# Kernel tuning notes

Hardware: AMD Instinct MI355X
Metric: run time of the kernel (lower is better)

The kernel has to match this reference:

```python
import jax, jax.numpy as jnp
import numpy as np

N, E, F_IN, H, D = 50000, 800000, 128, 4, 32


def setup_inputs() -> dict:
    key = jax.random.key(0)
    k_x, k_e, k_w, k_al, k_ar = jax.random.split(key, 5)
    x = jax.random.normal(k_x, (N, F_IN), dtype=jnp.float32)
    edge_index = jax.random.randint(k_e, (2, E), 0, N, dtype=jnp.int32).astype(jnp.int64)
    # xavier-uniform-like scales
    s_w = float(np.sqrt(6.0 / (F_IN + H * D)))
    s_a = float(np.sqrt(6.0 / (D + 1)))
    W = jax.random.uniform(k_w, (F_IN, H * D), jnp.float32, -s_w, s_w)
    att_l = jax.random.uniform(k_al, (H, D), jnp.float32, -s_a, s_a)
    att_r = jax.random.uniform(k_ar, (H, D), jnp.float32, -s_a, s_a)
    bias = jnp.zeros((H * D,), jnp.float32)
    return {"x": x, "edge_index": edge_index, "W": W, "att_l": att_l, "att_r": att_r, "bias": bias}


def reference(x, edge_index, W, att_l, att_r, bias):
    num_nodes = x.shape[0]
    n_heads, head_dim = att_l.shape
    h = (x @ W).reshape(num_nodes, n_heads, head_dim)          # [N,H,D]
    alpha_l = jnp.einsum('nhd,hd->nh', h, att_l)               # [N,H]
    alpha_r = jnp.einsum('nhd,hd->nh', h, att_r)               # [N,H]
    from_idx, to_idx = edge_index[0], edge_index[1]
    att = alpha_l[from_idx] + alpha_r[to_idx]                  # [E,H]
    att = jax.nn.leaky_relu(att, negative_slope=0.2)
    # segment softmax over edges grouped by destination node (shift by global
    # per-head max, exactly as the source's _softmax effectively does)
    att = att - jax.lax.stop_gradient(jnp.max(att, axis=0, keepdims=True))
    ex = jnp.exp(att)                                          # [E,H]
    denom = jax.ops.segment_sum(ex, to_idx, num_segments=num_nodes)  # [N,H]
    att_n = ex / (denom[to_idx] + 1e-9)                        # [E,H]
    # scatter-weighted aggregation: out[n] = sum_{e: to=n} att[e] * h[from[e]]
    msgs = att_n[:, :, None] * h[from_idx]                     # [E,H,D]
    out = jax.ops.segment_sum(msgs, to_idx, num_segments=num_nodes)  # [N,H,D]
    out = out.reshape(num_nodes, n_heads * head_dim) + bias
    return out
```

## Files before the change

kernel.cpp:

```cpp
#include <hip/hip_runtime.h>
#include <cstdint>

#define N_NODES 50000
#define N_EDGES 800000
#define F_IN    128
#define N_HEADS 4
#define HEAD_DIM 32
#define F_OUT   128

#define NBUCK   196
#define KA_GRID 256
#define EPB     (N_EDGES / KA_GRID)
#define CAPA    64
#define STAGE_CAP 6144

typedef unsigned int uint32;
typedef unsigned short ushort;
typedef __attribute__((ext_vector_type(8))) short short8v;
typedef __attribute__((ext_vector_type(4))) float float4v;

__device__ __forceinline__ ushort f2bf(float f) {
    uint32 u = __float_as_uint(f);
    return (ushort)((u + 0x7FFFu + ((u >> 16) & 1u)) >> 16);
}

__device__ __forceinline__ int block_scan_excl_256(int v, int* p_total)
{
    const int t = threadIdx.x, lane = t & 63, wv = t >> 6;
    int incl = v;
#pragma unroll
    for (int d = 1; d < 64; d <<= 1) {
        int u = __shfl_up(incl, d);
        if (lane >= d) incl += u;
    }
    __shared__ int wsum[4];
    if (lane == 63) wsum[wv] = incl;
    __syncthreads();
    int woff = 0;
#pragma unroll
    for (int j = 0; j < 4; ++j) {
        int s = wsum[j];
        if (j < wv) woff += s;
    }
    if (p_total) *p_total = wsum[0] + wsum[1] + wsum[2] + wsum[3];
    __syncthreads();
    return woff + incl - v;
}

__global__ __launch_bounds__(256) void k_bin(const int* __restrict__ ei,
    const float* __restrict__ W, ushort* __restrict__ WT_hi,
    ushort* __restrict__ WT_lo, uint2* __restrict__ priv, int* __restrict__ cnts)
{
    const int sb = blockIdx.x, t = threadIdx.x;

    const int id = sb * 256 + t;
    if (id < F_IN * F_OUT) {
        const int n = id & 127, k = id >> 7;
        const float w = W[k * F_OUT + n];
        const ushort hi = f2bf(w);
        const float hif = __uint_as_float((uint32)hi << 16);
        WT_hi[n * F_IN + k] = hi;
        WT_lo[n * F_IN + k] = f2bf(w - hif);
    }

    __shared__ int cur[NBUCK];
    if (t < NBUCK) cur[t] = 0;
    __syncthreads();

    const int e0 = sb * EPB;
    for (int i = t; i < EPB; i += 256) {
        const int from = ei[e0 + i];
        const int to   = ei[N_EDGES + e0 + i];
        const int b = to >> 8;
        const int slot = atomicAdd(&cur[b], 1);
        if (slot < CAPA)
            priv[((size_t)b * KA_GRID + sb) * CAPA + slot] =
                make_uint2((uint32)from, (uint32)to);
    }
    __syncthreads();
    if (t < NBUCK) cnts[t * KA_GRID + sb] = min(cur[t], CAPA);
}

__global__ __launch_bounds__(256) void k_bsum(const int* __restrict__ cnts,
                                              int* __restrict__ bsum)
{
    const int b = blockIdx.x, t = threadIdx.x;
    int v = cnts[b * KA_GRID + t];
#pragma unroll
    for (int d = 32; d; d >>= 1) v += __shfl_xor(v, d);
    __shared__ int ws[4];
    if ((t & 63) == 0) ws[t >> 6] = v;
    __syncthreads();
    if (t == 0) bsum[b] = ws[0] + ws[1] + ws[2] + ws[3];
}

__global__ __launch_bounds__(256) void k_scan_base(const int* __restrict__ bsum,
    int* __restrict__ bucket_base)
{
    const int t = threadIdx.x;
    int v = (t < NBUCK) ? bsum[t] : 0;
    const int ex = block_scan_excl_256(v, nullptr);
    if (t < NBUCK) bucket_base[t] = ex;
}

__global__ __launch_bounds__(256) void k_build(const uint2* __restrict__ priv,
    const int* __restrict__ cnts, const int* __restrict__ bucket_base,
    int* __restrict__ count, int* __restrict__ offsets, int* __restrict__ rec_from)
{
    __shared__ uint2 stage[STAGE_CAP];
    __shared__ int hist[256];
    __shared__ int curn[256];
    const int b = blockIdx.x, t = threadIdx.x;

    const int ct = cnts[b * KA_GRID + t];
    int total;
    const int so = block_scan_excl_256(ct, &total);

    const uint2* seg = priv + ((size_t)b * KA_GRID + t) * CAPA;
    if (so + ct <= STAGE_CAP)
        for (int i = 0; i < ct; ++i) stage[so + i] = seg[i];
    hist[t] = 0;
    __syncthreads();

    const int S = min(total, STAGE_CAP);
    for (int i = t; i < S; i += 256) atomicAdd(&hist[stage[i].y & 255], 1);
    __syncthreads();

    const int hv = hist[t];
    int tot2;
    const int lo = block_scan_excl_256(hv, &tot2);
    const int base = bucket_base[b];
    const int n = b * 256 + t;
    if (n < N_NODES) {
        count[n]   = hv;
        offsets[n] = base + lo;
    }
    curn[t] = lo;
    __syncthreads();

    for (int i = t; i < S; i += 256) {
        const uint2 e = stage[i];
        const int pos = atomicAdd(&curn[e.y & 255], 1);
        rec_from[base + pos] = (int)e.x;
    }
}

__global__ __launch_bounds__(256) void k_gemm_mfma(
    const float* __restrict__ x,
    const ushort* __restrict__ WT_hi, const ushort* __restrict__ WT_lo,
    const float* __restrict__ attl, const float* __restrict__ attr,
    uint32* __restrict__ hbp, float* __restrict__ aLp, float* __restrict__ aRp)
{
    const int lane = threadIdx.x & 63;
    const int wv   = threadIdx.x >> 6;
    const int q    = lane >> 4;
    const int c15  = lane & 15;
    const int row0 = blockIdx.x * 64 + wv * 16;
    if (row0 >= N_NODES) return;

    const float* xrow = x + (size_t)(row0 + c15) * F_IN + q * 8;
    short8v ahi[4], alo[4];
#pragma unroll
    for (int kt = 0; kt < 4; ++kt) {
        const float4 f0 = *(const float4*)(xrow + kt * 32);
        const float4 f1 = *(const float4*)(xrow + kt * 32 + 4);
        const float fs[8] = {f0.x, f0.y, f0.z, f0.w, f1.x, f1.y, f1.z, f1.w};
#pragma unroll
        for (int j = 0; j < 8; ++j) {
            const ushort hi = f2bf(fs[j]);
            const float hif = __uint_as_float((uint32)hi << 16);
            ahi[kt][j] = (short)hi;
            alo[kt][j] = (short)f2bf(fs[j] - hif);
        }
    }

    float4v acc[8];
#pragma unroll
    for (int nt = 0; nt < 8; ++nt) {
        float4v a = {0.f, 0.f, 0.f, 0.f};
        const ushort* bh_base = WT_hi + ((nt * 16 + c15) << 7) + q * 8;
        const ushort* bl_base = WT_lo + ((nt * 16 + c15) << 7) + q * 8;
#pragma unroll
        for (int kt = 0; kt < 4; ++kt) {
            const short8v bh = *(const short8v*)(bh_base + kt * 32);
            const short8v bl = *(const short8v*)(bl_base + kt * 32);
            a = __builtin_amdgcn_mfma_f32_16x16x32_bf16(ahi[kt], bh, a, 0, 0, 0);
            a = __builtin_amdgcn_mfma_f32_16x16x32_bf16(alo[kt], bh, a, 0, 0, 0);
            a = __builtin_amdgcn_mfma_f32_16x16x32_bf16(ahi[kt], bl, a, 0, 0, 0);
        }
        acc[nt] = a;
    }

#pragma unroll
    for (int nt = 0; nt < 4; ++nt) {
#pragma unroll
        for (int r = 0; r < 4; ++r) {
            const uint32 d = (uint32)f2bf(acc[nt][r]) | ((uint32)f2bf(acc[nt + 4][r]) << 16);
            hbp[(size_t)(row0 + q * 4 + r) * 64 + nt * 16 + c15] = d;
        }
    }

    float aLacc[4][4] = {{0.f}}, aRacc[4][4] = {{0.f}};
#pragma unroll
    for (int nt = 0; nt < 8; ++nt) {
        const float alv = attl[nt * 16 + c15];
        const float arv = attr[nt * 16 + c15];
        const int hh = nt >> 1;
#pragma unroll
        for (int r = 0; r < 4; ++r) {
            aLacc[r][hh] = fmaf(acc[nt][r], alv, aLacc[r][hh]);
            aRacc[r][hh] = fmaf(acc[nt][r], arv, aRacc[r][hh]);
        }
    }
#pragma unroll
    for (int r = 0; r < 4; ++r) {
#pragma unroll
        for (int hh = 0; hh < 4; ++hh) {
            float vl = aLacc[r][hh], vr = aRacc[r][hh];
#pragma unroll
            for (int d = 1; d < 16; d <<= 1) {
                vl += __shfl_xor(vl, d);
                vr += __shfl_xor(vr, d);
            }
            if (c15 == hh) {
                const int row = row0 + q * 4 + r;
                const int pos = (hh & 1) * 2 + (hh >> 1);
                aLp[row * N_HEADS + pos] = vl;
                aRp[row * N_HEADS + pos] = vr;
            }
        }
    }
}

__global__ __launch_bounds__(256) void k_agg(const int* __restrict__ rec_from,
    const int* __restrict__ count, const int* __restrict__ offsets,
    const float* __restrict__ aLp, const float* __restrict__ aRp,
    const uint32* __restrict__ hbp,
    const float* __restrict__ bias, float* __restrict__ out)
{
    const int lane = threadIdx.x & 63;
    const int n = blockIdx.x * 4 + (threadIdx.x >> 6);
    if (n >= N_NODES) return;
    const int cnt  = count[n];
    const int off  = offsets[n];
    const int hsel = (lane >> 5) * 2;
    const int l31  = lane & 31;
    const int gsel = lane & 32;
    const float2 arv = *(const float2*)&aRp[n * N_HEADS + hsel];
    float ax = 0.f, ay = 0.f, ds0 = 0.f, ds1 = 0.f;

    for (int base = 0; base < cnt; base += 32) {
        const int m = min(32, cnt - base);
        int vf = 0;
        float e0p = 0.f, e1p = 0.f;
        if (l31 < m) {
            vf = rec_from[off + base + l31];
            const float2 af = *(const float2*)&aLp[vf * N_HEADS + hsel];
            float t0 = af.x + arv.x; t0 = (t0 > 0.f) ? t0 : 0.2f * t0;
            float t1 = af.y + arv.y; t1 = (t1 > 0.f) ? t1 : 0.2f * t1;
            e0p = __expf(t0);
            e1p = __expf(t1);
        }
        int i = 0;
        for (; i + 4 <= m; i += 4) {
            const int s0 = gsel | i, s1 = gsel | (i + 1);
            const int s2 = gsel | (i + 2), s3 = gsel | (i + 3);
            const int f0 = __shfl(vf, s0), f1 = __shfl(vf, s1);
            const int f2i = __shfl(vf, s2), f3 = __shfl(vf, s3);
            const uint32 h0 = hbp[(size_t)f0 * 64 + lane];
            const uint32 h1 = hbp[(size_t)f1 * 64 + lane];
            const uint32 h2 = hbp[(size_t)f2i * 64 + lane];
            const uint32 h3 = hbp[(size_t)f3 * 64 + lane];
            const float e00 = __shfl(e0p, s0), e10 = __shfl(e1p, s0);
            const float e01 = __shfl(e0p, s1), e11 = __shfl(e1p, s1);
            const float e02 = __shfl(e0p, s2), e12 = __shfl(e1p, s2);
            const float e03 = __shfl(e0p, s3), e13 = __shfl(e1p, s3);
            ax = fmaf(e00, __uint_as_float(h0 << 16), ax);
            ay = fmaf(e10, __uint_as_float(h0 & 0xFFFF0000u), ay);
            ds0 += e00; ds1 += e10;
            ax = fmaf(e01, __uint_as_float(h1 << 16), ax);
            ay = fmaf(e11, __uint_as_float(h1 & 0xFFFF0000u), ay);
            ds0 += e01; ds1 += e11;
            ax = fmaf(e02, __uint_as_float(h2 << 16), ax);
            ay = fmaf(e12, __uint_as_float(h2 & 0xFFFF0000u), ay);
            ds0 += e02; ds1 += e12;
            ax = fmaf(e03, __uint_as_float(h3 << 16), ax);
            ay = fmaf(e13, __uint_as_float(h3 & 0xFFFF0000u), ay);
            ds0 += e03; ds1 += e13;
        }
        for (; i < m; ++i) {
            const int s = gsel | i;
            const int f = __shfl(vf, s);
            const uint32 hv = hbp[(size_t)f * 64 + lane];
            const float e0 = __shfl(e0p, s), e1 = __shfl(e1p, s);
            ax = fmaf(e0, __uint_as_float(hv << 16), ax);
            ay = fmaf(e1, __uint_as_float(hv & 0xFFFF0000u), ay);
            ds0 += e0; ds1 += e1;
        }
    }
    const float inv0 = 1.0f / (ds0 + 1e-9f);
    const float inv1 = 1.0f / (ds1 + 1e-9f);
    out[n * F_OUT + lane]      = ax * inv0 + bias[lane];
    out[n * F_OUT + 64 + lane] = ay * inv1 + bias[64 + lane];
}

extern "C" void kernel_launch(void* const* d_in, const int* in_sizes, int n_in,
                              void* d_out, int out_size, void* d_ws, size_t ws_size,
                              hipStream_t stream)
{
    const float* x    = (const float*)d_in[0];
    const int*   ei   = (const int*)d_in[1];
    const float* W    = (const float*)d_in[2];
    const float* attl = (const float*)d_in[3];
    const float* attr = (const float*)d_in[4];
    const float* bias = (const float*)d_in[5];
    float* out = (float*)d_out;

    char* p = (char*)d_ws;
    auto carve = [&](size_t bytes) -> char* {
        char* q = p;
        p += (bytes + 255) & ~size_t(255);
        return q;
    };
    uint32* hbp       = (uint32*)carve((size_t)N_NODES * 64 * 4);
    uint2*  priv      = (uint2*)carve((size_t)NBUCK * KA_GRID * CAPA * 8);
    int*    rec_from  = (int*)carve((size_t)N_EDGES * 4);
    ushort* WT_hi     = (ushort*)carve((size_t)F_IN * F_OUT * 2);
    ushort* WT_lo     = (ushort*)carve((size_t)F_IN * F_OUT * 2);
    float*  aLp       = (float*)carve((size_t)N_NODES * N_HEADS * 4);
    float*  aRp       = (float*)carve((size_t)N_NODES * N_HEADS * 4);
    int*    cnts      = (int*)carve((size_t)NBUCK * KA_GRID * 4);
    int*    bsum      = (int*)carve(NBUCK * 4);
    int*    bucket_base = (int*)carve(NBUCK * 4);
    int*    count     = (int*)carve((size_t)N_NODES * 4);
    int*    offsets   = (int*)carve((size_t)N_NODES * 4);

    k_bin<<<KA_GRID, 256, 0, stream>>>(ei, W, WT_hi, WT_lo, priv, cnts);
    k_bsum<<<NBUCK, 256, 0, stream>>>(cnts, bsum);
    k_scan_base<<<1, 256, 0, stream>>>(bsum, bucket_base);
    k_build<<<NBUCK, 256, 0, stream>>>(priv, cnts, bucket_base,
                                       count, offsets, rec_from);
    k_gemm_mfma<<<(N_NODES + 63) / 64, 256, 0, stream>>>(x, WT_hi, WT_lo,
                                                         attl, attr, hbp, aLp, aRp);
    k_agg<<<(N_NODES + 3) / 4, 256, 0, stream>>>(rec_from, count, offsets,
                                                 aLp, aRp, hbp, bias, out);
}
```

Baseline: 181.3 us.

## Split GEMM column halves across waves, coalesce staging copy, repack h layout

In k_build, the per-thread serial copy of each private edge segment into shared memory becomes a block-strided loop, so consecutive threads read consecutive priv entries and the loads coalesce. The GEMM kernel now gives each 16-row strip to two waves, each computing half the output columns (two heads). This doubles the grid and halves accumulator registers per wave. The packed bf16 h layout changes to match, and the aggregation kernel's output indexing and the attention-logit slot order are adjusted to fit. The cost is that each x strip is loaded and converted twice and there is more index arithmetic.

```diff
diff --git a/kernel.cpp b/kernel.cpp
--- a/kernel.cpp
+++ b/kernel.cpp
@@ -110,16 +110,27 @@
     __shared__ uint2 stage[STAGE_CAP];
     __shared__ int hist[256];
     __shared__ int curn[256];
+    __shared__ int so_s[256];
+    __shared__ int cts_s[256];
     const int b = blockIdx.x, t = threadIdx.x;
 
     const int ct = cnts[b * KA_GRID + t];
     int total;
     const int so = block_scan_excl_256(ct, &total);
-
-    const uint2* seg = priv + ((size_t)b * KA_GRID + t) * CAPA;
-    if (so + ct <= STAGE_CAP)
-        for (int i = 0; i < ct; ++i) stage[so + i] = seg[i];
+    so_s[t] = so;
+    cts_s[t] = ct;
     hist[t] = 0;
+    __syncthreads();
+
+    const uint2* pbase = priv + (size_t)b * KA_GRID * CAPA;
+    for (int idx = t; idx < KA_GRID * CAPA; idx += 256) {
+        const int sb = idx >> 6;
+        const int sl = idx & (CAPA - 1);
+        if (sl < cts_s[sb]) {
+            const int p = so_s[sb] + sl;
+            if (p < STAGE_CAP) stage[p] = pbase[idx];
+        }
+    }
     __syncthreads();
 
     const int S = min(total, STAGE_CAP);
@@ -149,13 +160,15 @@
     const float* __restrict__ x,
     const ushort* __restrict__ WT_hi, const ushort* __restrict__ WT_lo,
     const float* __restrict__ attl, const float* __restrict__ attr,
-    uint32* __restrict__ hbp, float* __restrict__ aLp, float* __restrict__ aRp)
-{
-    const int lane = threadIdx.x & 63;
-    const int wv   = threadIdx.x >> 6;
-    const int q    = lane >> 4;
-    const int c15  = lane & 15;
-    const int row0 = blockIdx.x * 64 + wv * 16;
+    uint32* __restrict__ hbq, float* __restrict__ aLp, float* __restrict__ aRp)
+{
+    const int lane  = threadIdx.x & 63;
+    const int wv    = threadIdx.x >> 6;
+    const int strip = blockIdx.x * 2 + (wv >> 1);
+    const int half  = wv & 1;
+    const int q     = lane >> 4;
+    const int c15   = lane & 15;
+    const int row0  = strip * 16;
     if (row0 >= N_NODES) return;
 
     const float* xrow = x + (size_t)(row0 + c15) * F_IN + q * 8;
@@ -174,9 +187,10 @@
         }
     }
 
-    float4v acc[8];
-#pragma unroll
-    for (int nt = 0; nt < 8; ++nt) {
+    float4v acc[4];
+#pragma unroll
+    for (int j = 0; j < 4; ++j) {
+        const int nt = half * 4 + j;
         float4v a = {0.f, 0.f, 0.f, 0.f};
         const ushort* bh_base = WT_hi + ((nt * 16 + c15) << 7) + q * 8;
         const ushort* bl_base = WT_lo + ((nt * 16 + c15) << 7) + q * 8;
@@ -188,45 +202,45 @@
             a = __builtin_amdgcn_mfma_f32_16x16x32_bf16(alo[kt], bh, a, 0, 0, 0);
             a = __builtin_amdgcn_mfma_f32_16x16x32_bf16(ahi[kt], bl, a, 0, 0, 0);
         }
-        acc[nt] = a;
-    }
-
-#pragma unroll
-    for (int nt = 0; nt < 4; ++nt) {
+        acc[j] = a;
+    }
+
+#pragma unroll
+    for (int j = 0; j < 2; ++j) {
 #pragma unroll
         for (int r = 0; r < 4; ++r) {
-            const uint32 d = (uint32)f2bf(acc[nt][r]) | ((uint32)f2bf(acc[nt + 4][r]) << 16);
-            hbp[(size_t)(row0 + q * 4 + r) * 64 + nt * 16 + c15] = d;
-        }
-    }
-
-    float aLacc[4][4] = {{0.f}}, aRacc[4][4] = {{0.f}};
-#pragma unroll
-    for (int nt = 0; nt < 8; ++nt) {
-        const float alv = attl[nt * 16 + c15];
-        const float arv = attr[nt * 16 + c15];
-        const int hh = nt >> 1;
+            const uint32 d = (uint32)f2bf(acc[j][r]) | ((uint32)f2bf(acc[j + 2][r]) << 16);
+            hbq[(size_t)(row0 + q * 4 + r) * 64 + half * 32 + j * 16 + c15] = d;
+        }
+    }
+
+    float aLacc[4][2] = {{0.f}}, aRacc[4][2] = {{0.f}};
+#pragma unroll
+    for (int j = 0; j < 4; ++j) {
+        const int col = (half * 4 + j) * 16 + c15;
+        const float alv = attl[col];
+        const float arv = attr[col];
+        const int hl = j >> 1;
 #pragma unroll
         for (int r = 0; r < 4; ++r) {
-            aLacc[r][hh] = fmaf(acc[nt][r], alv, aLacc[r][hh]);
-            aRacc[r][hh] = fmaf(acc[nt][r], arv, aRacc[r][hh]);
+            aLacc[r][hl] = fmaf(acc[j][r], alv, aLacc[r][hl]);
+            aRacc[r][hl] = fmaf(acc[j][r], arv, aRacc[r][hl]);
         }
     }
 #pragma unroll
     for (int r = 0; r < 4; ++r) {
 #pragma unroll
-        for (int hh = 0; hh < 4; ++hh) {
-            float vl = aLacc[r][hh], vr = aRacc[r][hh];
+        for (int hl = 0; hl < 2; ++hl) {
+            float vl = aLacc[r][hl], vr = aRacc[r][hl];
 #pragma unroll
             for (int d = 1; d < 16; d <<= 1) {
                 vl += __shfl_xor(vl, d);
                 vr += __shfl_xor(vr, d);
             }
-            if (c15 == hh) {
+            if (c15 == hl) {
                 const int row = row0 + q * 4 + r;
-                const int pos = (hh & 1) * 2 + (hh >> 1);
-                aLp[row * N_HEADS + pos] = vl;
-                aRp[row * N_HEADS + pos] = vr;
+                aLp[row * N_HEADS + half * 2 + hl] = vl;
+                aRp[row * N_HEADS + half * 2 + hl] = vr;
             }
         }
     }
@@ -235,7 +249,7 @@
 __global__ __launch_bounds__(256) void k_agg(const int* __restrict__ rec_from,
     const int* __restrict__ count, const int* __restrict__ offsets,
     const float* __restrict__ aLp, const float* __restrict__ aRp,
-    const uint32* __restrict__ hbp,
+    const uint32* __restrict__ hbq,
     const float* __restrict__ bias, float* __restrict__ out)
 {
     const int lane = threadIdx.x & 63;
@@ -267,10 +281,10 @@
             const int s2 = gsel | (i + 2), s3 = gsel | (i + 3);
             const int f0 = __shfl(vf, s0), f1 = __shfl(vf, s1);
             const int f2i = __shfl(vf, s2), f3 = __shfl(vf, s3);
-            const uint32 h0 = hbp[(size_t)f0 * 64 + lane];
-            const uint32 h1 = hbp[(size_t)f1 * 64 + lane];
-            const uint32 h2 = hbp[(size_t)f2i * 64 + lane];
-            const uint32 h3 = hbp[(size_t)f3 * 64 + lane];
+            const uint32 h0 = hbq[(size_t)f0 * 64 + lane];
+            const uint32 h1 = hbq[(size_t)f1 * 64 + lane];
+            const uint32 h2 = hbq[(size_t)f2i * 64 + lane];
+            const uint32 h3 = hbq[(size_t)f3 * 64 + lane];
             const float e00 = __shfl(e0p, s0), e10 = __shfl(e1p, s0);
             const float e01 = __shfl(e0p, s1), e11 = __shfl(e1p, s1);
             const float e02 = __shfl(e0p, s2), e12 = __shfl(e1p, s2);
@@ -291,7 +305,7 @@
         for (; i < m; ++i) {
             const int s = gsel | i;
             const int f = __shfl(vf, s);
-            const uint32 hv = hbp[(size_t)f * 64 + lane];
+            const uint32 hv = hbq[(size_t)f * 64 + lane];
             const float e0 = __shfl(e0p, s), e1 = __shfl(e1p, s);
             ax = fmaf(e0, __uint_as_float(hv << 16), ax);
             ay = fmaf(e1, __uint_as_float(hv & 0xFFFF0000u), ay);
@@ -300,8 +314,9 @@
     }
     const float inv0 = 1.0f / (ds0 + 1e-9f);
     const float inv1 = 1.0f / (ds1 + 1e-9f);
-    out[n * F_OUT + lane]      = ax * inv0 + bias[lane];
-    out[n * F_OUT + 64 + lane] = ay * inv1 + bias[64 + lane];
+    const int d0 = (lane < 32) ? lane : lane + 32;
+    out[n * F_OUT + d0]      = ax * inv0 + bias[d0];
+    out[n * F_OUT + d0 + 32] = ay * inv1 + bias[d0 + 32];
 }
 
 extern "C" void kernel_launch(void* const* d_in, const int* in_sizes, int n_in,
@@ -322,7 +337,7 @@
         p += (bytes + 255) & ~size_t(255);
         return q;
     };
-    uint32* hbp       = (uint32*)carve((size_t)N_NODES * 64 * 4);
+    uint32* hbq       = (uint32*)carve((size_t)N_NODES * 64 * 4);
     uint2*  priv      = (uint2*)carve((size_t)NBUCK * KA_GRID * CAPA * 8);
     int*    rec_from  = (int*)carve((size_t)N_EDGES * 4);
     ushort* WT_hi     = (ushort*)carve((size_t)F_IN * F_OUT * 2);
@@ -340,8 +355,8 @@
     k_scan_base<<<1, 256, 0, stream>>>(bsum, bucket_base);
     k_build<<<NBUCK, 256, 0, stream>>>(priv, cnts, bucket_base,
                                        count, offsets, rec_from);
-    k_gemm_mfma<<<(N_NODES + 63) / 64, 256, 0, stream>>>(x, WT_hi, WT_lo,
-                                                         attl, attr, hbp, aLp, aRp);
+    k_gemm_mfma<<<(N_NODES + 31) / 32, 256, 0, stream>>>(x, WT_hi, WT_lo,
+                                                         attl, attr, hbq, aLp, aRp);
     k_agg<<<(N_NODES + 3) / 4, 256, 0, stream>>>(rec_from, count, offsets,
-                                                 aLp, aRp, hbp, bias, out);
-}
+                                                 aLp, aRp, hbq, bias, out);
+}
```

Result: slower. 195.4 us (+7.8%).
